# Kernel optimization log

Hardware: AMD Instinct MI355X
Metric: run time of the kernel (lower is better)

The kernel has to match this reference:

```python
import jax, jax.numpy as jnp
import numpy as np

NUM_HEADS = 8

def setup_inputs() -> dict:
    key = jax.random.key(0)
    k1, k2, k3, k4, k5 = jax.random.split(key, 5)
    B, N, C = 4, 2048, 512
    x = jax.random.normal(k1, (B, N, C), dtype=jnp.float32)
    s = 1.0 / np.sqrt(C)
    qkv_w = jax.random.uniform(k2, (3 * C, C), dtype=jnp.float32, minval=-s, maxval=s)
    qkv_b = jax.random.uniform(k3, (3 * C,), dtype=jnp.float32, minval=-s, maxval=s)
    proj_w = jax.random.uniform(k4, (C, C), dtype=jnp.float32, minval=-s, maxval=s)
    proj_b = jax.random.uniform(k5, (C,), dtype=jnp.float32, minval=-s, maxval=s)
    return {"x": x, "qkv_w": qkv_w, "qkv_b": qkv_b, "proj_w": proj_w, "proj_b": proj_b}

def reference(x, qkv_w, qkv_b, proj_w, proj_b):
    B, N, C = x.shape
    H = NUM_HEADS
    D = C // H
    scale = D ** -0.5
    # qkv: [B,N,3C] -> [3,B,H,N,D]
    qkv = (jnp.einsum('bnc,oc->bno', x, qkv_w) + qkv_b)
    qkv = qkv.reshape(B, N, 3, H, D).transpose(2, 0, 3, 1, 4)
    q, k, v = qkv[0], qkv[1], qkv[2]
    attn = jnp.einsum('bhnd,bhmd->bhnm', q, k) * scale  # [B,H,N,N]
    attn = jax.nn.softmax(attn, axis=-1)
    out = jnp.einsum('bhnm,bhmd->bhnd', attn, v)  # [B,H,N,D]
    out = out.transpose(0, 2, 1, 3).reshape(B, N, C)
    return jnp.einsum('bnc,oc->bno', out, proj_w) + proj_b
```

## Files before the change

### kernel.cpp

```cpp
#include <hip/hip_runtime.h>
#include <stdint.h>


typedef short bf16x8 __attribute__((ext_vector_type(8)));
typedef float f32x2  __attribute__((ext_vector_type(2)));
typedef float f32x4  __attribute__((ext_vector_type(4)));
typedef float f32x16 __attribute__((ext_vector_type(16)));
typedef unsigned int u32x4 __attribute__((ext_vector_type(4)));

__device__ __forceinline__ unsigned short f2bf(float f) {
    unsigned int u = __builtin_bit_cast(unsigned int, f);
    u += 0x7fffu + ((u >> 16) & 1u);
    return (unsigned short)(u >> 16);
}
__device__ __forceinline__ unsigned int pk2(float a, float b) {
    return (unsigned int)f2bf(a) | ((unsigned int)f2bf(b) << 16);
}
__device__ __forceinline__ float fexp2(float x) {
    return __builtin_amdgcn_exp2f(x);
}
__device__ __forceinline__ bf16x8 ld8_f32(const float* __restrict__ p) {
    float4 f0 = *(const float4*)p;
    float4 f1 = *(const float4*)(p + 4);
    u32x4 u = {pk2(f0.x, f0.y), pk2(f0.z, f0.w), pk2(f1.x, f1.y), pk2(f1.z, f1.w)};
    return __builtin_bit_cast(bf16x8, u);
}
__device__ __forceinline__ void async16(const void* g, void* l) {
    __builtin_amdgcn_global_load_lds(
        (const __attribute__((address_space(1))) unsigned int*)g,
        (__attribute__((address_space(3))) unsigned int*)l,
        16, 0, 0);
}

#define MFMA16(a, b, c) __builtin_amdgcn_mfma_f32_16x16x32_bf16((a), (b), (c), 0, 0, 0)
#define MFMA32(a, b, c) __builtin_amdgcn_mfma_f32_32x32x16_bf16((a), (b), (c), 0, 0, 0)

__global__ void cvt_bf16(const float* __restrict__ x,
                         const float* __restrict__ w,
                         const float* __restrict__ w2,
                         unsigned short* __restrict__ xb,
                         unsigned short* __restrict__ wb,
                         unsigned short* __restrict__ wb2)
{
    const int G = 524288 + 98304 + 32768;
    for (int idx = blockIdx.x * 256 + threadIdx.x; idx < G; idx += gridDim.x * 256) {
        if (idx < 524288)
            *(bf16x8*)(xb + (size_t)idx * 8) = ld8_f32(x + (size_t)idx * 8);
        else if (idx < 524288 + 98304) {
            int j = idx - 524288;
            *(bf16x8*)(wb + (size_t)j * 8) = ld8_f32(w + (size_t)j * 8);
        } else {
            int j = idx - 524288 - 98304;
            *(bf16x8*)(wb2 + (size_t)j * 8) = ld8_f32(w2 + (size_t)j * 8);
        }
    }
}

__global__ __launch_bounds__(256, 4)
void gemm_qkv(const unsigned short* __restrict__ A,
              const unsigned short* __restrict__ B,
              const float* __restrict__ bias,
              unsigned short* __restrict__ out0,
              unsigned short* __restrict__ out1,
              unsigned short* __restrict__ out2,
              int K)
{
    __shared__ unsigned short sA[128 * 32];
    __shared__ unsigned short sB[128 * 32];

    const int tid  = threadIdx.x;
    const int wave = tid >> 6, lane = tid & 63;
    const int l = lane & 15, q16 = lane >> 4;
    const int wm = wave >> 1, wn = wave & 1;
    const int bid = blockIdx.x;
    const int slot = bid >> 3;
    const int m0 = ((bid & 7) * 8 + slot / 12) * 128;
    const int n0 = (slot % 12) * 128;

    f32x4 acc[4][4];
#pragma unroll
    for (int i = 0; i < 4; ++i)
#pragma unroll
        for (int j = 0; j < 4; ++j)
            acc[i][j] = (f32x4){0.f, 0.f, 0.f, 0.f};

    for (int k0 = 0; k0 < K; k0 += 32) {
#pragma unroll
        for (int call = 0; call < 2; ++call) {
            int L = call * 256 + tid;
            int r = L >> 2, c = L & 3;
            async16(A + (size_t)(m0 + r) * K + k0 + c * 8, sA + L * 8);
            async16(B + (size_t)(n0 + r) * K + k0 + c * 8, sB + L * 8);
        }
        __syncthreads();

        bf16x8 af[4], bfr[4];
#pragma unroll
        for (int i = 0; i < 4; ++i)
            af[i] = *(const bf16x8*)(sA + ((wm * 64 + i * 16 + l) * 4 + q16) * 8);
#pragma unroll
        for (int j = 0; j < 4; ++j)
            bfr[j] = *(const bf16x8*)(sB + ((wn * 64 + j * 16 + l) * 4 + q16) * 8);
#pragma unroll
        for (int i = 0; i < 4; ++i)
#pragma unroll
            for (int j = 0; j < 4; ++j)
                acc[i][j] = MFMA16(af[i], bfr[j], acc[i][j]);
        __syncthreads();
    }

    const float lscale = 0.18033688f;
#pragma unroll
    for (int i = 0; i < 4; ++i) {
#pragma unroll
        for (int j = 0; j < 4; ++j) {
            int col = n0 + wn * 64 + j * 16 + l;
            float bv = bias[col];
#pragma unroll
            for (int r = 0; r < 4; ++r) {
                int row = m0 + wm * 64 + i * 16 + q16 * 4 + r;
                float val = acc[i][j][r] + bv;
                int which = col >> 9;
                int h = (col >> 6) & 7, d = col & 63;
                int b = row >> 11, n = row & 2047;
                if (which == 0)
                    out0[(size_t)(((b * 8 + h) * 2048) + n) * 64 + d] = f2bf(val * lscale);
                else if (which == 1)
                    out1[(size_t)(((b * 8 + h) * 2048) + n) * 64 + d] = f2bf(val);
                else {
                    int np = (n & ~12) | ((n & 8) >> 1) | ((n & 4) << 1);
                    out2[(size_t)(((b * 8 + h) * 64) + d) * 2048 + np] = f2bf(val);
                }
            }
        }
    }
}

__global__ __launch_bounds__(256, 4)
void gemm_out(const unsigned short* __restrict__ A,
              const unsigned short* __restrict__ B,
              const float* __restrict__ bias,
              float* __restrict__ outf,
              int K, int N)
{
    __shared__ unsigned short sA[64 * 32];
    __shared__ unsigned short sB[128 * 32];

    const int tid  = threadIdx.x;
    const int wave = tid >> 6, lane = tid & 63;
    const int l = lane & 15, q16 = lane >> 4;
    const int wm = wave >> 1, wn = wave & 1;
    const int bid = blockIdx.x;
    const int slot = bid >> 3;
    const int m0 = ((bid & 7) * 16 + (slot >> 2)) * 64;
    const int n0 = (slot & 3) * 128;

    f32x4 acc[2][4];
#pragma unroll
    for (int i = 0; i < 2; ++i)
#pragma unroll
        for (int j = 0; j < 4; ++j)
            acc[i][j] = (f32x4){0.f, 0.f, 0.f, 0.f};

    for (int k0 = 0; k0 < K; k0 += 32) {
        {
            int r = tid >> 2, c = tid & 3;
            async16(A + (size_t)(m0 + r) * K + k0 + c * 8, sA + tid * 8);
        }
#pragma unroll
        for (int call = 0; call < 2; ++call) {
            int L = call * 256 + tid;
            int r = L >> 2, c = L & 3;
            async16(B + (size_t)(n0 + r) * K + k0 + c * 8, sB + L * 8);
        }
        __syncthreads();

        bf16x8 af[2], bfr[4];
#pragma unroll
        for (int i = 0; i < 2; ++i)
            af[i] = *(const bf16x8*)(sA + ((wm * 32 + i * 16 + l) * 4 + q16) * 8);
#pragma unroll
        for (int j = 0; j < 4; ++j)
            bfr[j] = *(const bf16x8*)(sB + ((wn * 64 + j * 16 + l) * 4 + q16) * 8);
#pragma unroll
        for (int i = 0; i < 2; ++i)
#pragma unroll
            for (int j = 0; j < 4; ++j)
                acc[i][j] = MFMA16(af[i], bfr[j], acc[i][j]);
        __syncthreads();
    }

#pragma unroll
    for (int i = 0; i < 2; ++i) {
#pragma unroll
        for (int j = 0; j < 4; ++j) {
            int col = n0 + wn * 64 + j * 16 + l;
            float bv = bias[col];
#pragma unroll
            for (int r = 0; r < 4; ++r) {
                int row = m0 + wm * 32 + i * 16 + q16 * 4 + r;
                outf[(size_t)row * N + col] = acc[i][j][r] + bv;
            }
        }
    }
}

__global__ __launch_bounds__(512, 2)
void attn_fused(const unsigned short* __restrict__ Q,
                const unsigned short* __restrict__ Km,
                const unsigned short* __restrict__ Vt,
                unsigned short* __restrict__ O)
{
    __shared__ unsigned short sAll[49152];

    const int tid  = threadIdx.x;
    const int wave = tid >> 6, lane = tid & 63;
    const int l31 = lane & 31, h = lane >> 5;
    const int swz = l31 & 7;
    const int qq = wave >> 1, kh = wave & 1;
    const int bid = blockIdx.x;
    const int slot = bid >> 3;
    const int bh = (bid & 7) * 4 + (slot >> 3);
    const int qc = slot & 7;
    const int q0 = qc * 256 + qq * 64;

    const unsigned short* Kp = Km + (size_t)bh * 2048 * 64;
    const unsigned short* Vp = Vt + (size_t)bh * 64 * 2048;
    unsigned short* sKf = sAll;
    unsigned short* sVf = sAll + 24576;

    int ka[4], va[2][2];
#pragma unroll
    for (int ks = 0; ks < 4; ++ks)
        ka[ks] = (kh * 64 + l31) * 64 + ((ks * 2 + h) ^ swz) * 8;
#pragma unroll
    for (int m1 = 0; m1 < 2; ++m1)
#pragma unroll
        for (int ks2 = 0; ks2 < 2; ++ks2)
            va[m1][ks2] = l31 * 128 + ((m1 * 4 + ks2 * 2 + h) ^ swz) * 8 + kh * 64;

    int ksrc[2], vsrc[2], dsl[2];
#pragma unroll
    for (int c = 0; c < 2; ++c) {
        int s = c * 512 + tid;
        int rk = s >> 3;
        ksrc[c] = rk * 64 + ((s & 7) ^ (rk & 7)) * 8;
        int rv = s >> 4;
        vsrc[c] = rv * 2048 + ((s & 15) ^ (rv & 7)) * 8;
        dsl[c] = s * 8;
    }

    bf16x8 qf[2][4];
#pragma unroll
    for (int qt = 0; qt < 2; ++qt)
#pragma unroll
        for (int ks = 0; ks < 4; ++ks)
            qf[qt][ks] = *(const bf16x8*)(Q + (size_t)(bh * 2048 + q0 + qt * 32 + l31) * 64
                                          + ks * 16 + h * 8);

    f32x16 oacc[2][2];
#pragma unroll
    for (int qt = 0; qt < 2; ++qt)
#pragma unroll
        for (int dt = 0; dt < 2; ++dt)
#pragma unroll
            for (int e = 0; e < 16; ++e) oacc[qt][dt][e] = 0.f;
    f32x16 Zv;
#pragma unroll
    for (int e = 0; e < 16; ++e) Zv[e] = 0.f;
    f32x2 l2[2];
    l2[0] = (f32x2){0.f, 0.f};
    l2[1] = (f32x2){0.f, 0.f};

#pragma unroll
    for (int c = 0; c < 2; ++c) {
        async16(Kp + ksrc[c], (void*)(sKf + dsl[c]));
        async16(Vp + vsrc[c], (void*)(sVf + dsl[c]));
    }
#pragma unroll
    for (int c = 0; c < 2; ++c) {
        async16(Kp + (size_t)128 * 64 + ksrc[c], (void*)(sKf + 8192 + dsl[c]));
        async16(Vp + (size_t)128 + vsrc[c], (void*)(sVf + 8192 + dsl[c]));
    }
    asm volatile("s_waitcnt vmcnt(4)" ::: "memory");
    __builtin_amdgcn_s_barrier();
    __builtin_amdgcn_sched_barrier(0);

    int off0 = 0, off1 = 8192, off2 = 16384;

    for (int it = 0; it < 16; ++it) {
        if (it < 14) {
            size_t kv = (size_t)(it + 2) * 128;
#pragma unroll
            for (int c = 0; c < 2; ++c) {
                async16(Kp + kv * 64 + ksrc[c], (void*)(sKf + off2 + dsl[c]));
                async16(Vp + kv + vsrc[c], (void*)(sVf + off2 + dsl[c]));
            }
        }

        const unsigned short* sKc = sKf + off0;
        const unsigned short* sVc = sVf + off0;
        f32x16 sacc[2][2];
#pragma unroll
        for (int mt = 0; mt < 2; ++mt) {
            bf16x8 kf0 = *(const bf16x8*)(sKc + ka[0] + mt * 2048);
            __builtin_amdgcn_s_setprio(1);
            sacc[0][mt] = MFMA32(kf0, qf[0][0], Zv);
            sacc[1][mt] = MFMA32(kf0, qf[1][0], Zv);
            __builtin_amdgcn_s_setprio(0);
#pragma unroll
            for (int ks = 1; ks < 4; ++ks) {
                bf16x8 kf = *(const bf16x8*)(sKc + ka[ks] + mt * 2048);
                __builtin_amdgcn_s_setprio(1);
                sacc[0][mt] = MFMA32(kf, qf[0][ks], sacc[0][mt]);
                sacc[1][mt] = MFMA32(kf, qf[1][ks], sacc[1][mt]);
                __builtin_amdgcn_s_setprio(0);
            }
        }

#pragma unroll
        for (int mt = 0; mt < 2; ++mt) {
            unsigned int pk[2][4][2];
#pragma unroll
            for (int qt = 0; qt < 2; ++qt) {
#pragma unroll
                for (int g = 0; g < 4; ++g) {
                    float p0 = fexp2(sacc[qt][mt][4 * g + 0]);
                    float p1 = fexp2(sacc[qt][mt][4 * g + 1]);
                    float p2 = fexp2(sacc[qt][mt][4 * g + 2]);
                    float p3 = fexp2(sacc[qt][mt][4 * g + 3]);
                    l2[qt] += (f32x2){p0, p1};
                    l2[qt] += (f32x2){p2, p3};
                    pk[qt][g][0] = __builtin_amdgcn_perm(
                        __builtin_bit_cast(unsigned int, p1),
                        __builtin_bit_cast(unsigned int, p0), 0x07060302u);
                    pk[qt][g][1] = __builtin_amdgcn_perm(
                        __builtin_bit_cast(unsigned int, p3),
                        __builtin_bit_cast(unsigned int, p2), 0x07060302u);
                }
            }
#pragma unroll
            for (int ks2 = 0; ks2 < 2; ++ks2) {
                u32x4 bu0, bu1;
                bu0[0] = pk[0][2 * ks2][0];
                bu0[1] = pk[0][2 * ks2][1];
                bu0[2] = pk[0][2 * ks2 + 1][0];
                bu0[3] = pk[0][2 * ks2 + 1][1];
                bu1[0] = pk[1][2 * ks2][0];
                bu1[1] = pk[1][2 * ks2][1];
                bu1[2] = pk[1][2 * ks2 + 1][0];
                bu1[3] = pk[1][2 * ks2 + 1][1];
                bf16x8 bf0 = __builtin_bit_cast(bf16x8, bu0);
                bf16x8 bf1 = __builtin_bit_cast(bf16x8, bu1);
#pragma unroll
                for (int dt = 0; dt < 2; ++dt) {
                    bf16x8 vf = *(const bf16x8*)(sVc + va[mt][ks2] + dt * 4096);
                    __builtin_amdgcn_s_setprio(1);
                    oacc[0][dt] = MFMA32(vf, bf0, oacc[0][dt]);
                    oacc[1][dt] = MFMA32(vf, bf1, oacc[1][dt]);
                    __builtin_amdgcn_s_setprio(0);
                }
            }
        }

        if (it < 14) {
            asm volatile("s_waitcnt vmcnt(4)" ::: "memory");
        } else if (it == 14) {
            asm volatile("s_waitcnt vmcnt(0)" ::: "memory");
        }
        if (it < 15) {
            asm volatile("s_waitcnt lgkmcnt(0)" ::: "memory");
            __builtin_amdgcn_s_barrier();
            __builtin_amdgcn_sched_barrier(0);
        }

        int t = off0; off0 = off1; off1 = off2; off2 = t;
    }

    __syncthreads();
    float* sf = (float*)sAll;
    float* sl = sf + 16384;
    if (kh == 1) {
        const int base = (qq * 64 + lane) * 64;
#pragma unroll
        for (int qt = 0; qt < 2; ++qt)
#pragma unroll
            for (int dt = 0; dt < 2; ++dt) {
                int chunk = (qt * 2 + dt) ^ (lane & 3);
                *(f32x16*)(sf + base + chunk * 16) = oacc[qt][dt];
            }
        *(f32x2*)(sl + (qq * 64 + lane) * 4 + 0) = l2[0];
        *(f32x2*)(sl + (qq * 64 + lane) * 4 + 2) = l2[1];
    }
    __syncthreads();
    if (kh == 0) {
        const int base = (qq * 64 + lane) * 64;
#pragma unroll
        for (int qt = 0; qt < 2; ++qt)
#pragma unroll
            for (int dt = 0; dt < 2; ++dt) {
                int chunk = (qt * 2 + dt) ^ (lane & 3);
                f32x16 part = *(const f32x16*)(sf + base + chunk * 16);
#pragma unroll
                for (int e = 0; e < 16; ++e) oacc[qt][dt][e] += part[e];
            }
        l2[0] += *(const f32x2*)(sl + (qq * 64 + lane) * 4 + 0);
        l2[1] += *(const f32x2*)(sl + (qq * 64 + lane) * 4 + 2);

        const int b = bh >> 3, hh = bh & 7;
#pragma unroll
        for (int qt = 0; qt < 2; ++qt) {
            float l_run = l2[qt][0] + l2[qt][1];
            l_run += __shfl_xor(l_run, 32);
            float inv = 1.f / fmaxf(l_run, 1e-20f);
            unsigned short* obase = O + ((size_t)(b * 2048 + q0 + qt * 32 + l31)) * 512 + hh * 64;
#pragma unroll
            for (int dt = 0; dt < 2; ++dt)
#pragma unroll
                for (int g = 0; g < 4; ++g) {
                    int d = dt * 32 + 8 * g + 4 * h;
                    unsigned int w0 = pk2(oacc[qt][dt][4 * g + 0] * inv,
                                          oacc[qt][dt][4 * g + 1] * inv);
                    unsigned int w1 = pk2(oacc[qt][dt][4 * g + 2] * inv,
                                          oacc[qt][dt][4 * g + 3] * inv);
                    uint2 w = {w0, w1};
                    *(uint2*)(obase + d) = w;
                }
        }
    }
}

extern "C" void kernel_launch(void* const* d_in, const int* in_sizes, int n_in,
                              void* d_out, int out_size, void* d_ws, size_t ws_size,
                              hipStream_t stream)
{
    const float* x      = (const float*)d_in[0];
    const float* qkv_w  = (const float*)d_in[1];
    const float* qkv_b  = (const float*)d_in[2];
    const float* proj_w = (const float*)d_in[3];
    const float* proj_b = (const float*)d_in[4];

    const size_t PER = 4u * 8u * 2048u * 64u;
    unsigned short* q_ws  = (unsigned short*)d_ws;
    unsigned short* k_ws  = q_ws  + PER;
    unsigned short* vt_ws = k_ws  + PER;
    unsigned short* ao_ws = vt_ws + PER;
    unsigned short* wb2   = ao_ws + PER;

    unsigned short* xb = (unsigned short*)d_out;
    unsigned short* wb = xb + PER;

    cvt_bf16<<<dim3(640), 256, 0, stream>>>(x, qkv_w, proj_w, xb, wb, wb2);
    gemm_qkv<<<dim3(768), 256, 0, stream>>>(xb, wb, qkv_b, q_ws, k_ws, vt_ws, 512);
    attn_fused<<<dim3(256), 512, 0, stream>>>(q_ws, k_ws, vt_ws, ao_ws);
    gemm_out<<<dim3(512), 256, 0, stream>>>(ao_ws, wb2, proj_b, (float*)d_out, 512, 512);
}
```

Measured before the change: 154.1 us.

## Software-pipeline next tile's QK^T with current softmax and PV

Splits each 128-key tile's score computation into two halves. The first half of the next tile's QK^T MFMAs is issued between the two softmax+PV stages of the current tile, so exp/pack VALU work can overlap with matrix-core work. To make this safe, the prologue and the per-iteration waits now drain all outstanding async loads (vmcnt(0)), which shortens the effective prefetch depth. The launch bounds also drop the two-blocks-per-CU hint, which may let register use grow and reduce occupancy.

```diff
diff --git a/kernel.cpp b/kernel.cpp
--- a/kernel.cpp
+++ b/kernel.cpp
@@ -205,7 +205,7 @@
     }
 }
 
-__global__ __launch_bounds__(512, 2)
+__global__ __launch_bounds__(512)
 void attn_fused(const unsigned short* __restrict__ Q,
                 const unsigned short* __restrict__ Km,
                 const unsigned short* __restrict__ Vt,
@@ -272,6 +272,62 @@
     l2[0] = (f32x2){0.f, 0.f};
     l2[1] = (f32x2){0.f, 0.f};
 
+    f32x16 sA0, sA1, sB0, sB1;
+
+    auto softmax_pv = [&](const f32x16& s0, const f32x16& s1, int mt,
+                          const unsigned short* sVc) {
+        unsigned int pk0[4][2], pk1[4][2];
+#pragma unroll
+        for (int g = 0; g < 4; ++g) {
+            float a0 = fexp2(s0[4 * g + 0]);
+            float a1 = fexp2(s0[4 * g + 1]);
+            float a2 = fexp2(s0[4 * g + 2]);
+            float a3 = fexp2(s0[4 * g + 3]);
+            l2[0] += (f32x2){a0, a1};
+            l2[0] += (f32x2){a2, a3};
+            pk0[g][0] = __builtin_amdgcn_perm(
+                __builtin_bit_cast(unsigned int, a1),
+                __builtin_bit_cast(unsigned int, a0), 0x07060302u);
+            pk0[g][1] = __builtin_amdgcn_perm(
+                __builtin_bit_cast(unsigned int, a3),
+                __builtin_bit_cast(unsigned int, a2), 0x07060302u);
+            float b0 = fexp2(s1[4 * g + 0]);
+            float b1 = fexp2(s1[4 * g + 1]);
+            float b2 = fexp2(s1[4 * g + 2]);
+            float b3 = fexp2(s1[4 * g + 3]);
+            l2[1] += (f32x2){b0, b1};
+            l2[1] += (f32x2){b2, b3};
+            pk1[g][0] = __builtin_amdgcn_perm(
+                __builtin_bit_cast(unsigned int, b1),
+                __builtin_bit_cast(unsigned int, b0), 0x07060302u);
+            pk1[g][1] = __builtin_amdgcn_perm(
+                __builtin_bit_cast(unsigned int, b3),
+                __builtin_bit_cast(unsigned int, b2), 0x07060302u);
+        }
+#pragma unroll
+        for (int ks2 = 0; ks2 < 2; ++ks2) {
+            u32x4 bu0, bu1;
+            bu0[0] = pk0[2 * ks2][0];
+            bu0[1] = pk0[2 * ks2][1];
+            bu0[2] = pk0[2 * ks2 + 1][0];
+            bu0[3] = pk0[2 * ks2 + 1][1];
+            bu1[0] = pk1[2 * ks2][0];
+            bu1[1] = pk1[2 * ks2][1];
+            bu1[2] = pk1[2 * ks2 + 1][0];
+            bu1[3] = pk1[2 * ks2 + 1][1];
+            bf16x8 bf0 = __builtin_bit_cast(bf16x8, bu0);
+            bf16x8 bf1 = __builtin_bit_cast(bf16x8, bu1);
+#pragma unroll
+            for (int dt = 0; dt < 2; ++dt) {
+                bf16x8 vf = *(const bf16x8*)(sVc + va[mt][ks2] + dt * 4096);
+                __builtin_amdgcn_s_setprio(1);
+                oacc[0][dt] = MFMA32(vf, bf0, oacc[0][dt]);
+                oacc[1][dt] = MFMA32(vf, bf1, oacc[1][dt]);
+                __builtin_amdgcn_s_setprio(0);
+            }
+        }
+    };
+
 #pragma unroll
     for (int c = 0; c < 2; ++c) {
         async16(Kp + ksrc[c], (void*)(sKf + dsl[c]));
@@ -282,99 +338,76 @@
         async16(Kp + (size_t)128 * 64 + ksrc[c], (void*)(sKf + 8192 + dsl[c]));
         async16(Vp + (size_t)128 + vsrc[c], (void*)(sVf + 8192 + dsl[c]));
     }
-    asm volatile("s_waitcnt vmcnt(4)" ::: "memory");
+    asm volatile("s_waitcnt vmcnt(0)" ::: "memory");
     __builtin_amdgcn_s_barrier();
     __builtin_amdgcn_sched_barrier(0);
+    {
+        bf16x8 kf = *(const bf16x8*)(sKf + ka[0]);
+        sA0 = MFMA32(kf, qf[0][0], Zv);
+        sA1 = MFMA32(kf, qf[1][0], Zv);
+#pragma unroll
+        for (int ks = 1; ks < 4; ++ks) {
+            kf = *(const bf16x8*)(sKf + ka[ks]);
+            sA0 = MFMA32(kf, qf[0][ks], sA0);
+            sA1 = MFMA32(kf, qf[1][ks], sA1);
+        }
+    }
 
     int off0 = 0, off1 = 8192, off2 = 16384;
 
-    for (int it = 0; it < 16; ++it) {
-        if (it < 14) {
-            size_t kv = (size_t)(it + 2) * 128;
+    for (int t = 0; t < 16; ++t) {
+        const unsigned short* sKc = sKf + off0;
+        const unsigned short* sVc = sVf + off0;
+
+        if (t < 14) {
+            size_t kv = (size_t)(t + 2) * 128;
 #pragma unroll
             for (int c = 0; c < 2; ++c) {
                 async16(Kp + kv * 64 + ksrc[c], (void*)(sKf + off2 + dsl[c]));
                 async16(Vp + kv + vsrc[c], (void*)(sVf + off2 + dsl[c]));
             }
         }
-
-        const unsigned short* sKc = sKf + off0;
-        const unsigned short* sVc = sVf + off0;
-        f32x16 sacc[2][2];
-#pragma unroll
-        for (int mt = 0; mt < 2; ++mt) {
-            bf16x8 kf0 = *(const bf16x8*)(sKc + ka[0] + mt * 2048);
+        {
+            bf16x8 kf = *(const bf16x8*)(sKc + ka[0] + 2048);
             __builtin_amdgcn_s_setprio(1);
-            sacc[0][mt] = MFMA32(kf0, qf[0][0], Zv);
-            sacc[1][mt] = MFMA32(kf0, qf[1][0], Zv);
+            sB0 = MFMA32(kf, qf[0][0], Zv);
+            sB1 = MFMA32(kf, qf[1][0], Zv);
             __builtin_amdgcn_s_setprio(0);
 #pragma unroll
             for (int ks = 1; ks < 4; ++ks) {
-                bf16x8 kf = *(const bf16x8*)(sKc + ka[ks] + mt * 2048);
+                kf = *(const bf16x8*)(sKc + ka[ks] + 2048);
                 __builtin_amdgcn_s_setprio(1);
-                sacc[0][mt] = MFMA32(kf, qf[0][ks], sacc[0][mt]);
-                sacc[1][mt] = MFMA32(kf, qf[1][ks], sacc[1][mt]);
+                sB0 = MFMA32(kf, qf[0][ks], sB0);
+                sB1 = MFMA32(kf, qf[1][ks], sB1);
                 __builtin_amdgcn_s_setprio(0);
             }
         }
-
-#pragma unroll
-        for (int mt = 0; mt < 2; ++mt) {
-            unsigned int pk[2][4][2];
-#pragma unroll
-            for (int qt = 0; qt < 2; ++qt) {
-#pragma unroll
-                for (int g = 0; g < 4; ++g) {
-                    float p0 = fexp2(sacc[qt][mt][4 * g + 0]);
-                    float p1 = fexp2(sacc[qt][mt][4 * g + 1]);
-                    float p2 = fexp2(sacc[qt][mt][4 * g + 2]);
-                    float p3 = fexp2(sacc[qt][mt][4 * g + 3]);
-                    l2[qt] += (f32x2){p0, p1};
-                    l2[qt] += (f32x2){p2, p3};
-                    pk[qt][g][0] = __builtin_amdgcn_perm(
-                        __builtin_bit_cast(unsigned int, p1),
-                        __builtin_bit_cast(unsigned int, p0), 0x07060302u);
-                    pk[qt][g][1] = __builtin_amdgcn_perm(
-                        __builtin_bit_cast(unsigned int, p3),
-                        __builtin_bit_cast(unsigned int, p2), 0x07060302u);
-                }
-            }
-#pragma unroll
-            for (int ks2 = 0; ks2 < 2; ++ks2) {
-                u32x4 bu0, bu1;
-                bu0[0] = pk[0][2 * ks2][0];
-                bu0[1] = pk[0][2 * ks2][1];
-                bu0[2] = pk[0][2 * ks2 + 1][0];
-                bu0[3] = pk[0][2 * ks2 + 1][1];
-                bu1[0] = pk[1][2 * ks2][0];
-                bu1[1] = pk[1][2 * ks2][1];
-                bu1[2] = pk[1][2 * ks2 + 1][0];
-                bu1[3] = pk[1][2 * ks2 + 1][1];
-                bf16x8 bf0 = __builtin_bit_cast(bf16x8, bu0);
-                bf16x8 bf1 = __builtin_bit_cast(bf16x8, bu1);
-#pragma unroll
-                for (int dt = 0; dt < 2; ++dt) {
-                    bf16x8 vf = *(const bf16x8*)(sVc + va[mt][ks2] + dt * 4096);
-                    __builtin_amdgcn_s_setprio(1);
-                    oacc[0][dt] = MFMA32(vf, bf0, oacc[0][dt]);
-                    oacc[1][dt] = MFMA32(vf, bf1, oacc[1][dt]);
-                    __builtin_amdgcn_s_setprio(0);
-                }
-            }
-        }
-
-        if (it < 14) {
-            asm volatile("s_waitcnt vmcnt(4)" ::: "memory");
-        } else if (it == 14) {
-            asm volatile("s_waitcnt vmcnt(0)" ::: "memory");
-        }
-        if (it < 15) {
-            asm volatile("s_waitcnt lgkmcnt(0)" ::: "memory");
+        softmax_pv(sA0, sA1, 0, sVc);
+
+        if (t < 15) {
+            const unsigned short* sKn = sKf + off1;
+            bf16x8 kf = *(const bf16x8*)(sKn + ka[0]);
+            __builtin_amdgcn_s_setprio(1);
+            sA0 = MFMA32(kf, qf[0][0], Zv);
+            sA1 = MFMA32(kf, qf[1][0], Zv);
+            __builtin_amdgcn_s_setprio(0);
+#pragma unroll
+            for (int ks = 1; ks < 4; ++ks) {
+                kf = *(const bf16x8*)(sKn + ka[ks]);
+                __builtin_amdgcn_s_setprio(1);
+                sA0 = MFMA32(kf, qf[0][ks], sA0);
+                sA1 = MFMA32(kf, qf[1][ks], sA1);
+                __builtin_amdgcn_s_setprio(0);
+            }
+        }
+        softmax_pv(sB0, sB1, 1, sVc);
+
+        if (t < 15) {
+            asm volatile("s_waitcnt vmcnt(0) lgkmcnt(0)" ::: "memory");
             __builtin_amdgcn_s_barrier();
             __builtin_amdgcn_sched_barrier(0);
         }
-
-        int t = off0; off0 = off1; off1 = off2; off2 = t;
+        int tmp = off0; off0 = off1; off1 = off2; off2 = tmp;
     }
 
     __syncthreads();
```

New measurement: 155.5 us. Within noise of the previous version (+0.9%).
